# Performance work log

Hardware: AMD Instinct MI355X
Metric: run time of the kernel (lower is better)

The kernel has to match this reference:

```python
import jax, jax.numpy as jnp
import numpy as np

EPS = 1e-12  # torch F.normalize clamps the norm at eps


def diff_sign(x):
    # straight-through estimator: forward = sign (-1/+1), backward = identity
    sign = 2.0 * (x >= 0).astype(x.dtype) - 1.0
    return x + jax.lax.stop_gradient(sign - x)


def setup_inputs() -> dict:
    key = jax.random.key(0)
    k0, k1, k2 = jax.random.split(key, 3)
    B, H, W, C = 64, 32, 32, 512
    bits = 16
    x = jax.random.normal(k0, (B, H, W, C), dtype=jnp.float32)
    # torch Linear init: U(-1/sqrt(fan_in), 1/sqrt(fan_in)); exact dist irrelevant for correctness
    s1 = 1.0 / np.sqrt(C)
    Wp = jax.random.uniform(k1, (C, bits), jnp.float32, -s1, s1)
    bp = jnp.zeros((bits,), jnp.float32)
    s2 = 1.0 / np.sqrt(bits)
    Wr = jax.random.uniform(k2, (bits, C), jnp.float32, -s2, s2)
    br = jnp.zeros((C,), jnp.float32)
    return {"x": x, "Wp": Wp, "bp": bp, "Wr": Wr, "br": br}


def reference(x, Wp, bp, Wr, br):
    B, H, W, C = x.shape
    t = x.reshape(B, H * W, C)                      # [B, HW, C]
    z = jnp.einsum('btc,cd->btd', t, Wp) + bp       # [B, HW, bits]
    norm = jnp.sqrt(jnp.sum(z * z, axis=-1, keepdims=True))
    z = z / jnp.maximum(norm, EPS)                  # F.normalize(p=2, dim=-1)
    code = diff_sign(z).reshape(B, H, W, -1)        # [B, H, W, bits]
    recon = jnp.einsum('bhwd,dc->bhwc', code, Wr) + br
    return recon
```

## Files before the change

kernel.cpp:

```cpp
#include <hip/hip_runtime.h>
#include <stdint.h>


#define ROWS   65536
#define TILE   16
#define BLOCKS (ROWS / TILE)
#define TAU    1e-3f

#define BAR()    asm volatile("s_waitcnt lgkmcnt(0)\n\ts_barrier" ::: "memory")
#define WAITV(N) asm volatile("s_waitcnt vmcnt(" #N ")" ::: "memory")
#define WAITL()  asm volatile("s_waitcnt lgkmcnt(0)" ::: "memory")
#define CFENCE() asm volatile("" ::: "memory")

typedef const __attribute__((address_space(1))) void* gas1_t;
typedef __attribute__((address_space(3))) void*       las3_t;
typedef float v2f __attribute__((ext_vector_type(2)));

__global__ __launch_bounds__(256, 2)
void bsq_fused(const float* __restrict__ x,
               const float* __restrict__ Wp,
               const float* __restrict__ bp,
               const float* __restrict__ Wr,
               const float* __restrict__ br,
               float* __restrict__ out)
{
    const int tid = threadIdx.x;
    const int w   = tid >> 6;
    const int l   = tid & 63;
    const int cg  = l >> 4;
    const int dg  = l & 15;

    __shared__ __align__(16) float  xl[4 * 1024];
    __shared__ __align__(16) float  zp[TILE][16][4];
    __shared__ __align__(16) double zb64[4][16];

    v2f wpA[8], wpB[8];
#pragma unroll
    for (int j = 0; j < 8; ++j) {
        const float* wj = Wp + (w * 128 + j * 16 + cg * 4) * 16 + dg;
        wpA[j] = (v2f){ wj[0],  wj[16] };
        wpB[j] = (v2f){ wj[32], wj[48] };
    }
    const float bpf = bp[dg];

    const int row0 = blockIdx.x * TILE;
    const float* xsrc = x + (size_t)row0 * 512 + (size_t)(l >> 5) * 512
                          + w * 128 + (l & 31) * 4;

    auto stage = [&](int s) {
        __builtin_amdgcn_global_load_lds(
            (gas1_t)(xsrc + (size_t)(2 * s) * 512),
            (las3_t)(&xl[(s & 3) * 1024 + w * 256]), 16, 0, 0);
    };

    auto dot_part = [&](int s, int p, v2f& accA, v2f& accB) {
        const float* bx = &xl[(s & 3) * 1024 + w * 256 + p * 128 + cg * 4];
        float4 xr[8];
#pragma unroll
        for (int j = 0; j < 8; ++j) xr[j] = *(const float4*)(bx + j * 16);
        accA = (v2f){0.f, 0.f};  accB = (v2f){0.f, 0.f};
#pragma unroll
        for (int j = 0; j < 8; ++j) {
            accA += (v2f){ xr[j].x, xr[j].y } * wpA[j];
            accB += (v2f){ xr[j].z, xr[j].w } * wpB[j];
        }
    };
    auto fin_part = [&](int r, v2f accA, v2f accB) {
        float a = (accA.x + accA.y) + (accB.x + accB.y);
        a += __shfl_xor(a, 16, 64);
        a += __shfl_xor(a, 32, 64);
        if (l < 16) zp[r][l][w] = a;
    };

#pragma unroll
    for (int s = 0; s < 4; ++s) stage(s);
    WAITV(0);

#pragma unroll 1
    for (int c = 0; c < 4; ++c) {
        v2f aA0, aB0, aA1, aB1;
        dot_part(c, 0, aA0, aB0);
        dot_part(c, 1, aA1, aB1);
        CFENCE();
        WAITL();
        stage(c + 4);
        CFENCE();
        fin_part(2 * c, aA0, aB0);
        fin_part(2 * c + 1, aA1, aB1);
    }
    BAR();

    v2f wrv[16];
    const float2* Wr2 = (const float2*)Wr;
#pragma unroll
    for (int d = 0; d < 16; ++d) {
        const float2 t = Wr2[d * 256 + tid];
        wrv[d] = (v2f){ t.x, t.y };
    }
    const float2 brt = ((const float2*)br)[tid];
    const v2f br2v = (v2f){ brt.x, brt.y };
    WAITV(0);

    uint32_t amb = 0;
    auto recon_row = [&](int r) {
        const float4 q = *(const float4*)&zp[r][dg][0];
        const float  z = (q.x + q.y) + (q.z + q.w) + bpf;
        if (__ballot(fabsf(z) < TAU)) amb |= (1u << r);
        const int m = (int)(__ballot(z >= 0.0f) & 0xFFFFull);
        v2f o = br2v;
#pragma unroll
        for (int d = 0; d < 16; ++d) {
            const float s = ((m >> d) & 1) ? 1.0f : -1.0f;
            o += (v2f){ s, s } * wrv[d];
        }
        ((float2*)out)[(size_t)(row0 + r) * 256 + tid] = make_float2(o.x, o.y);
    };

#pragma unroll 1
    for (int c = 4; c < 8; ++c) {
        v2f aA0, aB0, aA1, aB1;
        dot_part(c, 0, aA0, aB0);
        dot_part(c, 1, aA1, aB1);
        fin_part(2 * c, aA0, aB0);
        fin_part(2 * c + 1, aA1, aB1);
        recon_row(2 * (c - 4));
        recon_row(2 * (c - 4) + 1);
    }
    BAR();

#pragma unroll 2
    for (int r = 8; r < TILE; ++r) recon_row(r);

    const double bpd = (double)bpf;
#pragma unroll 1
    while (amb) {
        const int rr = __ffs(amb) - 1;
        amb &= amb - 1;
        const int row = row0 + rr;

        const float* xp = x + (size_t)row * 512 + w * 128 + cg * 4;
        double ad = 0.0;
#pragma unroll
        for (int j = 0; j < 8; ++j) {
            const float4 xf = *(const float4*)(xp + j * 16);
#pragma unroll
            for (int e = 0; e < 4; ++e) {
                const float wpe = Wp[(w * 128 + j * 16 + cg * 4 + e) * 16 + dg];
                const float xe  = e == 0 ? xf.x : e == 1 ? xf.y
                               : e == 2 ? xf.z : xf.w;
                ad = fma((double)xe, (double)wpe, ad);
            }
        }
        ad += __shfl_xor(ad, 16, 64);
        ad += __shfl_xor(ad, 32, 64);
        if (l < 16) zb64[w][l] = ad;
        BAR();
        const double zd = (zb64[0][dg] + zb64[1][dg])
                        + (zb64[2][dg] + zb64[3][dg]) + bpd;
        const int m = (int)(__ballot(zd >= 0.0) & 0xFFFFull);
        BAR();

        v2f o = br2v;
#pragma unroll
        for (int d = 0; d < 16; ++d) {
            const float s = ((m >> d) & 1) ? 1.0f : -1.0f;
            o += (v2f){ s, s } * wrv[d];
        }
        ((float2*)out)[(size_t)row * 256 + tid] = make_float2(o.x, o.y);
    }
}

extern "C" void kernel_launch(void* const* d_in, const int* in_sizes, int n_in,
                              void* d_out, int out_size, void* d_ws, size_t ws_size,
                              hipStream_t stream) {
    const float* x  = (const float*)d_in[0];
    const float* Wp = (const float*)d_in[1];
    const float* bp = (const float*)d_in[2];
    const float* Wr = (const float*)d_in[3];
    const float* br = (const float*)d_in[4];
    float* out = (float*)d_out;

    bsq_fused<<<BLOCKS, 256, 0, stream>>>(x, Wp, bp, Wr, br, out);
}
```

Measured before the change: 63.81 us.

## Process 64 rows per block with a three-bank software pipeline

Each block now handles 64 rows instead of 16, which cuts the grid to a quarter of its former size. The Wp and Wr weight loads into registers are paid once per 64 rows, and the Wr loads now happen before the x stream starts. Projection results rotate through three shared-memory banks, so reconstruction of one 8-row group overlaps the staged x loads and dot products of the next group, with finer vmcnt waits. The risks are fewer blocks to spread across CUs, which hurts tail balance, and more intricate wait counting, where a mistake could read incomplete shared-memory data.

```diff
diff --git a/kernel.cpp b/kernel.cpp
--- a/kernel.cpp
+++ b/kernel.cpp
@@ -3,8 +3,8 @@
 
 
 #define ROWS   65536
-#define TILE   16
-#define BLOCKS (ROWS / TILE)
+#define RPB    64
+#define BLOCKS (ROWS / RPB)
 #define TAU    1e-3f
 
 #define BAR()    asm volatile("s_waitcnt lgkmcnt(0)\n\ts_barrier" ::: "memory")
@@ -31,7 +31,7 @@
     const int dg  = l & 15;
 
     __shared__ __align__(16) float  xl[4 * 1024];
-    __shared__ __align__(16) float  zp[TILE][16][4];
+    __shared__ __align__(16) float  zp[3][8][16][4];
     __shared__ __align__(16) double zb64[4][16];
 
     v2f wpA[8], wpB[8];
@@ -43,7 +43,17 @@
     }
     const float bpf = bp[dg];
 
-    const int row0 = blockIdx.x * TILE;
+    v2f wrv[16];
+    const float2* Wr2 = (const float2*)Wr;
+#pragma unroll
+    for (int d = 0; d < 16; ++d) {
+        const float2 t = Wr2[d * 256 + tid];
+        wrv[d] = (v2f){ t.x, t.y };
+    }
+    const float2 brt = ((const float2*)br)[tid];
+    const v2f br2v = (v2f){ brt.x, brt.y };
+
+    const int row0 = blockIdx.x * RPB;
     const float* xsrc = x + (size_t)row0 * 512 + (size_t)(l >> 5) * 512
                           + w * 128 + (l & 31) * 4;
 
@@ -65,47 +75,30 @@
             accB += (v2f){ xr[j].z, xr[j].w } * wpB[j];
         }
     };
-    auto fin_part = [&](int r, v2f accA, v2f accB) {
+    auto fin_part = [&](int bank, int rg, v2f accA, v2f accB) {
         float a = (accA.x + accA.y) + (accB.x + accB.y);
         a += __shfl_xor(a, 16, 64);
         a += __shfl_xor(a, 32, 64);
-        if (l < 16) zp[r][l][w] = a;
+        if (l < 16) zp[bank][rg][l][w] = a;
     };
 
-#pragma unroll
-    for (int s = 0; s < 4; ++s) stage(s);
-    WAITV(0);
-
-#pragma unroll 1
-    for (int c = 0; c < 4; ++c) {
+    auto chunk = [&](int s, int bank, int rg, bool do_stage) {
         v2f aA0, aB0, aA1, aB1;
-        dot_part(c, 0, aA0, aB0);
-        dot_part(c, 1, aA1, aB1);
+        dot_part(s, 0, aA0, aB0);
+        dot_part(s, 1, aA1, aB1);
         CFENCE();
         WAITL();
-        stage(c + 4);
+        if (do_stage) stage(s + 4);
         CFENCE();
-        fin_part(2 * c, aA0, aB0);
-        fin_part(2 * c + 1, aA1, aB1);
-    }
-    BAR();
+        fin_part(bank, rg,     aA0, aB0);
+        fin_part(bank, rg + 1, aA1, aB1);
+    };
 
-    v2f wrv[16];
-    const float2* Wr2 = (const float2*)Wr;
-#pragma unroll
-    for (int d = 0; d < 16; ++d) {
-        const float2 t = Wr2[d * 256 + tid];
-        wrv[d] = (v2f){ t.x, t.y };
-    }
-    const float2 brt = ((const float2*)br)[tid];
-    const v2f br2v = (v2f){ brt.x, brt.y };
-    WAITV(0);
-
-    uint32_t amb = 0;
-    auto recon_row = [&](int r) {
-        const float4 q = *(const float4*)&zp[r][dg][0];
+    unsigned long long amb = 0ull;
+    auto recon_row = [&](int bank, int rg, int r) {
+        const float4 q = *(const float4*)&zp[bank][rg][dg][0];
         const float  z = (q.x + q.y) + (q.z + q.w) + bpf;
-        if (__ballot(fabsf(z) < TAU)) amb |= (1u << r);
+        if (__ballot(fabsf(z) < TAU)) amb |= (1ull << r);
         const int m = (int)(__ballot(z >= 0.0f) & 0xFFFFull);
         v2f o = br2v;
 #pragma unroll
@@ -116,25 +109,47 @@
         ((float2*)out)[(size_t)(row0 + r) * 256 + tid] = make_float2(o.x, o.y);
     };
 
-#pragma unroll 1
-    for (int c = 4; c < 8; ++c) {
-        v2f aA0, aB0, aA1, aB1;
-        dot_part(c, 0, aA0, aB0);
-        dot_part(c, 1, aA1, aB1);
-        fin_part(2 * c, aA0, aB0);
-        fin_part(2 * c + 1, aA1, aB1);
-        recon_row(2 * (c - 4));
-        recon_row(2 * (c - 4) + 1);
-    }
+#pragma unroll
+    for (int s = 0; s < 4; ++s) stage(s);
+    WAITV(0);
+
+#pragma unroll
+    for (int c = 0; c < 4; ++c) chunk(c, 0, 2 * c, true);
     BAR();
 
-#pragma unroll 2
-    for (int r = 8; r < TILE; ++r) recon_row(r);
+#pragma unroll
+    for (int c = 0; c < 4; ++c) { WAITV(3); chunk(4 + c, 1, 2 * c, true); }
+    BAR();
+#pragma unroll
+    for (int rg = 0; rg < 8; ++rg) recon_row(0, rg, rg);
+
+#pragma unroll 1
+    for (int g = 2; g < 7; ++g) {
+        const int bank = g % 3, pbank = (g - 1) % 3;
+#pragma unroll
+        for (int c = 0; c < 4; ++c) {
+            WAITV(11);
+            chunk(4 * g + c, bank, 2 * c, true);
+        }
+        BAR();
+#pragma unroll
+        for (int rg = 0; rg < 8; ++rg) recon_row(pbank, rg, 8 * (g - 1) + rg);
+    }
+
+    WAITV(11); chunk(28, 1, 0, false);
+    WAITV(10); chunk(29, 1, 2, false);
+    WAITV(9);  chunk(30, 1, 4, false);
+    WAITV(8);  chunk(31, 1, 6, false);
+    BAR();
+#pragma unroll
+    for (int rg = 0; rg < 8; ++rg) recon_row(0, rg, 48 + rg);
+#pragma unroll
+    for (int rg = 0; rg < 8; ++rg) recon_row(1, rg, 56 + rg);
 
     const double bpd = (double)bpf;
 #pragma unroll 1
     while (amb) {
-        const int rr = __ffs(amb) - 1;
+        const int rr = __ffsll(amb) - 1;
         amb &= amb - 1;
         const int row = row0 + rr;
 
```

Measured after the change: 77.09 us. 20.8% more time.

## Remap projection dot product to 4 outputs per lane with DPP/swizzle reduction

Applied to the files above, without the earlier changes.

Changes the thread-to-work mapping of the x·Wp projection so that each lane handles 16 channels for 4 output bits instead of 32 channels for one bit. This cuts LDS reads per lane from 8 float4 to 2 per row. The cross-lane reduction now uses a DPP transpose-reduce plus ds_swizzle in place of 64-wide shfl_xor. The ballot mask is repacked to match the new lane layout. Register use for Wp stays at 16 v2f, but the lane shuffling adds select and permute instructions.

```diff
diff --git a/kernel.cpp b/kernel.cpp
--- a/kernel.cpp
+++ b/kernel.cpp
@@ -11,6 +11,11 @@
 #define WAITV(N) asm volatile("s_waitcnt vmcnt(" #N ")" ::: "memory")
 #define WAITL()  asm volatile("s_waitcnt lgkmcnt(0)" ::: "memory")
 #define CFENCE() asm volatile("" ::: "memory")
+
+#define DPPF(v, CTRL) __int_as_float(__builtin_amdgcn_update_dpp( \
+    0, __float_as_int(v), CTRL, 0xF, 0xF, true))
+#define SWZF(v, OFF)  __int_as_float(__builtin_amdgcn_ds_swizzle( \
+    __float_as_int(v), OFF))
 
 typedef const __attribute__((address_space(1))) void* gas1_t;
 typedef __attribute__((address_space(3))) void*       las3_t;
@@ -27,6 +32,8 @@
     const int tid = threadIdx.x;
     const int w   = tid >> 6;
     const int l   = tid & 63;
+    const int cl  = l & 15;
+    const int dq  = l >> 4;
     const int cg  = l >> 4;
     const int dg  = l & 15;
 
@@ -34,14 +41,21 @@
     __shared__ __align__(16) float  zp[TILE][16][4];
     __shared__ __align__(16) double zb64[4][16];
 
-    v2f wpA[8], wpB[8];
-#pragma unroll
-    for (int j = 0; j < 8; ++j) {
-        const float* wj = Wp + (w * 128 + j * 16 + cg * 4) * 16 + dg;
-        wpA[j] = (v2f){ wj[0],  wj[16] };
-        wpB[j] = (v2f){ wj[32], wj[48] };
-    }
-    const float bpf = bp[dg];
+    const int ca = w * 128 + cl * 4;
+    const int db = dq * 4;
+    v2f wp2[4][4];
+#pragma unroll
+    for (int d = 0; d < 4; ++d) {
+#pragma unroll
+        for (int jj = 0; jj < 2; ++jj) {
+            const float* pa = Wp + (ca + 2 * jj) * 16 + db + d;
+            wp2[d][jj]     = (v2f){ pa[0], pa[16] };
+            const float* pb = Wp + (ca + 64 + 2 * jj) * 16 + db + d;
+            wp2[d][2 + jj] = (v2f){ pb[0], pb[16] };
+        }
+    }
+    const float bpr = bp[db + (l & 3)];
+    const double bpd = (double)bp[dg];
 
     const int row0 = blockIdx.x * TILE;
     const float* xsrc = x + (size_t)row0 * 512 + (size_t)(l >> 5) * 512
@@ -53,23 +67,35 @@
             (las3_t)(&xl[(s & 3) * 1024 + w * 256]), 16, 0, 0);
     };
 
-    auto dot_part = [&](int s, int p, v2f& accA, v2f& accB) {
-        const float* bx = &xl[(s & 3) * 1024 + w * 256 + p * 128 + cg * 4];
-        float4 xr[8];
-#pragma unroll
-        for (int j = 0; j < 8; ++j) xr[j] = *(const float4*)(bx + j * 16);
-        accA = (v2f){0.f, 0.f};  accB = (v2f){0.f, 0.f};
-#pragma unroll
-        for (int j = 0; j < 8; ++j) {
-            accA += (v2f){ xr[j].x, xr[j].y } * wpA[j];
-            accB += (v2f){ xr[j].z, xr[j].w } * wpB[j];
-        }
-    };
-    auto fin_part = [&](int r, v2f accA, v2f accB) {
-        float a = (accA.x + accA.y) + (accB.x + accB.y);
-        a += __shfl_xor(a, 16, 64);
-        a += __shfl_xor(a, 32, 64);
-        if (l < 16) zp[r][l][w] = a;
+    auto dot_part = [&](int s, int p, v2f (&acc)[4]) {
+        const float* bx = &xl[(s & 3) * 1024 + w * 256 + p * 128];
+        const float4 xr0 = *(const float4*)(bx + cl * 4);
+        const float4 xr1 = *(const float4*)(bx + 64 + cl * 4);
+        const v2f x0 = { xr0.x, xr0.y }, x1 = { xr0.z, xr0.w };
+        const v2f x2 = { xr1.x, xr1.y }, x3 = { xr1.z, xr1.w };
+#pragma unroll
+        for (int d = 0; d < 4; ++d) {
+            v2f a = x0 * wp2[d][0];
+            a += x1 * wp2[d][1];
+            a += x2 * wp2[d][2];
+            a += x3 * wp2[d][3];
+            acc[d] = a;
+        }
+    };
+
+    auto fin_part = [&](int r, v2f (&acc)[4]) {
+        const float v0 = acc[0].x + acc[0].y, v1 = acc[1].x + acc[1].y;
+        const float v2 = acc[2].x + acc[2].y, v3 = acc[3].x + acc[3].y;
+        const bool b0 = (l & 1), b1 = (l & 2);
+        const float g01 = b0 ? v0 : v1;
+        const float k01 = (b0 ? v1 : v0) + DPPF(g01, 0xB1);
+        const float g23 = b0 ? v2 : v3;
+        const float k23 = (b0 ? v3 : v2) + DPPF(g23, 0xB1);
+        const float g2  = b1 ? k01 : k23;
+        float z1 = (b1 ? k23 : k01) + DPPF(g2, 0x4E);
+        z1 += SWZF(z1, 0x101F);
+        z1 += SWZF(z1, 0x201F);
+        if ((l & 12) == 0) zp[r][db + (l & 3)][w] = z1;
     };
 
 #pragma unroll
@@ -78,15 +104,15 @@
 
 #pragma unroll 1
     for (int c = 0; c < 4; ++c) {
-        v2f aA0, aB0, aA1, aB1;
-        dot_part(c, 0, aA0, aB0);
-        dot_part(c, 1, aA1, aB1);
+        v2f a0[4], a1[4];
+        dot_part(c, 0, a0);
+        dot_part(c, 1, a1);
         CFENCE();
         WAITL();
         stage(c + 4);
         CFENCE();
-        fin_part(2 * c, aA0, aB0);
-        fin_part(2 * c + 1, aA1, aB1);
+        fin_part(2 * c, a0);
+        fin_part(2 * c + 1, a1);
     }
     BAR();
 
@@ -103,10 +129,13 @@
 
     uint32_t amb = 0;
     auto recon_row = [&](int r) {
-        const float4 q = *(const float4*)&zp[r][dg][0];
-        const float  z = (q.x + q.y) + (q.z + q.w) + bpf;
+        const int dl = db + (l & 3);
+        const float4 q = *(const float4*)&zp[r][dl][0];
+        const float  z = (q.x + q.y) + (q.z + q.w) + bpr;
         if (__ballot(fabsf(z) < TAU)) amb |= (1u << r);
-        const int m = (int)(__ballot(z >= 0.0f) & 0xFFFFull);
+        const unsigned long long bb = __ballot(z >= 0.0f);
+        const int m = (int)((bb & 0xFull) | ((bb >> 12) & 0xF0ull)
+                          | ((bb >> 24) & 0xF00ull) | ((bb >> 36) & 0xF000ull));
         v2f o = br2v;
 #pragma unroll
         for (int d = 0; d < 16; ++d) {
@@ -118,11 +147,11 @@
 
 #pragma unroll 1
     for (int c = 4; c < 8; ++c) {
-        v2f aA0, aB0, aA1, aB1;
-        dot_part(c, 0, aA0, aB0);
-        dot_part(c, 1, aA1, aB1);
-        fin_part(2 * c, aA0, aB0);
-        fin_part(2 * c + 1, aA1, aB1);
+        v2f a0[4], a1[4];
+        dot_part(c, 0, a0);
+        dot_part(c, 1, a1);
+        fin_part(2 * c, a0);
+        fin_part(2 * c + 1, a1);
         recon_row(2 * (c - 4));
         recon_row(2 * (c - 4) + 1);
     }
@@ -131,7 +160,6 @@
 #pragma unroll 2
     for (int r = 8; r < TILE; ++r) recon_row(r);
 
-    const double bpd = (double)bpf;
 #pragma unroll 1
     while (amb) {
         const int rr = __ffs(amb) - 1;
```

Result: slower. 67.51 us (+5.8%).
